# Kernel optimization log

Hardware: AMD Instinct MI355X
Metric: run time of the kernel (lower is better)

## Reference

```python
import jax, jax.numpy as jnp
import numpy as np

L, D, H, S, V, B = 8, 512, 8, 64, 66, 256
DH = D // H
EPS = 1e-10  # module's LayerNorm eps, added to std (not var)


def layernorm(x, g, b):
    # torch.std_mean default: unbiased std (ddof=1)
    mean = jnp.mean(x, axis=-1, keepdims=True)
    std = jnp.std(x, axis=-1, ddof=1, keepdims=True)
    return (x - mean) / (std + EPS) * g + b


def setup_inputs() -> dict:
    key = jax.random.key(0)
    ks = iter(jax.random.split(key, 32))
    def n(shape, scale=0.02):
        return jax.random.normal(next(ks), shape, dtype=jnp.float32) * scale
    return {
        "input_ids": jax.random.randint(next(ks), (B, S), 0, V),
        "targets": jax.random.randint(next(ks), (B, S), 0, V),
        "tok_emb": n((V, D), 1.0),
        "pos_emb": n((S, D), 1.0),
        "Wq": n((L, D, H, DH)), "Wk": n((L, D, H, DH)), "Wv": n((L, D, H, DH)),
        "Wo": n((L, D, D)), "bo": jnp.zeros((L, D), jnp.float32),
        "W1": n((L, D, 4 * D)), "b1": jnp.zeros((L, 4 * D), jnp.float32),
        "W2": n((L, 4 * D, D)), "b2": jnp.zeros((L, D), jnp.float32),
        "ln1_g": jnp.ones((L, D), jnp.float32), "ln1_b": jnp.zeros((L, D), jnp.float32),
        "ln2_g": jnp.ones((L, D), jnp.float32), "ln2_b": jnp.zeros((L, D), jnp.float32),
        "lnf_g": jnp.ones((D,), jnp.float32), "lnf_b": jnp.zeros((D,), jnp.float32),
        "Wu": n((D, V)), "bu": jnp.zeros((V,), jnp.float32),
    }


def reference(input_ids, targets, tok_emb, pos_emb, Wq, Wk, Wv, Wo, bo,
              W1, b1, W2, b2, ln1_g, ln1_b, ln2_g, ln2_b, lnf_g, lnf_b, Wu, bu):
    x = tok_emb[input_ids] + pos_emb[None, :, :]  # [B,S,D]
    scale = 1.0 / jnp.sqrt(jnp.float32(D))        # module scales by 1/sqrt(d_model)
    mask = jnp.tril(jnp.ones((S, S), dtype=bool))
    for l in range(L):
        h = layernorm(x, ln1_g[l], ln1_b[l])
        q = jnp.einsum('bsd,dhe->bhse', h, Wq[l])
        k = jnp.einsum('bsd,dhe->bhse', h, Wk[l])
        v = jnp.einsum('bsd,dhe->bhse', h, Wv[l])
        scores = jnp.einsum('bhse,bhte->bhst', q, k) * scale
        scores = jnp.where(mask, scores, -jnp.inf)
        attn = jax.nn.softmax(scores, axis=-1)
        o = jnp.einsum('bhst,bhte->bhse', attn, v)
        o = o.transpose(0, 2, 1, 3).reshape(B, S, D)  # concat heads (head order preserved)
        x = x + o @ Wo[l] + bo[l]
        h2 = layernorm(x, ln2_g[l], ln2_b[l])
        hid = jax.nn.gelu(h2 @ W1[l] + b1[l], approximate=False)  # nn.GELU exact
        x = x + hid @ W2[l] + b2[l]
    x = layernorm(x, lnf_g, lnf_b)
    logits = x @ Wu + bu  # [B,S,V]
    logp = jax.nn.log_softmax(logits, axis=-1)
    loss = -jnp.mean(jnp.take_along_axis(logp, targets[..., None], axis=-1))
    return logits, loss
```

## Files before the change

### kernel.cpp

```cpp
#include <hip/hip_runtime.h>
#include <hip/hip_bf16.h>
#include <math.h>

#define D_MODEL 512
#define NHEAD   8
#define DHEAD   64
#define SEQ     64
#define BATCH   256
#define NLAYER  8
#define VOCAB   66
#define FFDIM   2048
#define NTOK    (BATCH * SEQ)

typedef __attribute__((ext_vector_type(8))) short short8;
typedef __attribute__((ext_vector_type(4))) float f32x4;
typedef __attribute__((ext_vector_type(16))) float f32x16;

__device__ inline void async_copy16(const void* g, void* l) {
    __builtin_amdgcn_global_load_lds(
        (const __attribute__((address_space(1))) void*)g,
        (__attribute__((address_space(3))) void*)l,
        16, 0, 0);
}

__global__ __launch_bounds__(256) void transpose_conv(
        const float* __restrict__ W, __hip_bfloat16* __restrict__ Wt,
        int K, int M, size_t inLS, size_t outLS, int rowOff) {
    __shared__ float tile[32][33];
    int m0 = blockIdx.x * 32, k0 = blockIdx.y * 32;
    const float* Wl = W + blockIdx.z * inLS;
    __hip_bfloat16* Wtl = Wt + blockIdx.z * outLS;
    int t = threadIdx.x;
    #pragma unroll
    for (int p = 0; p < 4; p++) {
        int idx = t + p * 256;
        int kr = idx >> 5, mc = idx & 31;
        tile[kr][mc] = Wl[(size_t)(k0 + kr) * M + m0 + mc];
    }
    __syncthreads();
    #pragma unroll
    for (int p = 0; p < 4; p++) {
        int idx = t + p * 256;
        int mr = idx >> 5, kc = idx & 31;
        Wtl[(size_t)(rowOff + m0 + mr) * K + k0 + kc] = __float2bfloat16(tile[kc][mr]);
    }
}

__global__ __launch_bounds__(256) void conv_wu(
        const float* __restrict__ Wu, __hip_bfloat16* __restrict__ WuT) {
    int idx = blockIdx.x * 256 + threadIdx.x;
    int m = idx >> 9, k = idx & 511;
    WuT[idx] = __float2bfloat16(m < VOCAB ? Wu[(size_t)k * VOCAB + m] : 0.f);
}

__global__ void embed_kernel(const int* __restrict__ ids, const float* __restrict__ tok,
                             const float* __restrict__ pos, float* __restrict__ x) {
    int idx = blockIdx.x * 256 + threadIdx.x;
    int n = idx >> 9;
    int d = idx & 511;
    int s = n & (SEQ - 1);
    x[idx] = tok[ids[n] * D_MODEL + d] + pos[s * D_MODEL + d];
}

__global__ __launch_bounds__(256) void ln_kernel(
        const float* __restrict__ x, const float* __restrict__ g,
        const float* __restrict__ b, __hip_bfloat16* __restrict__ y) {
    int row = blockIdx.x * 4 + (threadIdx.x >> 6);
    int lane = threadIdx.x & 63;
    const float* xr = x + (size_t)row * D_MODEL + lane * 8;
    f32x4 v0 = *(const f32x4*)xr;
    f32x4 v1 = *(const f32x4*)(xr + 4);
    float s = 0.f, ss = 0.f;
    #pragma unroll
    for (int e = 0; e < 4; e++) { s += v0[e] + v1[e]; ss += v0[e] * v0[e] + v1[e] * v1[e]; }
    #pragma unroll
    for (int o = 1; o < 64; o <<= 1) {
        s  += __shfl_xor(s, o);
        ss += __shfl_xor(ss, o);
    }
    float mean = s / (float)D_MODEL;
    float var = (ss - (float)D_MODEL * mean * mean) / (float)(D_MODEL - 1);
    float denom = sqrtf(fmaxf(var, 0.f)) + 1e-10f;
    f32x4 g0 = *(const f32x4*)(g + lane * 8);
    f32x4 g1 = *(const f32x4*)(g + lane * 8 + 4);
    f32x4 b0 = *(const f32x4*)(b + lane * 8);
    f32x4 b1 = *(const f32x4*)(b + lane * 8 + 4);
    short8 outv;
    #pragma unroll
    for (int e = 0; e < 4; e++) {
        outv[e]     = ((__hip_bfloat16_raw)__float2bfloat16((v0[e] - mean) / denom * g0[e] + b0[e])).x;
        outv[e + 4] = ((__hip_bfloat16_raw)__float2bfloat16((v1[e] - mean) / denom * g1[e] + b1[e])).x;
    }
    *(short8*)((short*)y + (size_t)row * D_MODEL + lane * 8) = outv;
}

template <int ACT, int OUTMODE>
__global__ __launch_bounds__(256) void mfma_gemm(
        const __hip_bfloat16* __restrict__ A, const __hip_bfloat16* __restrict__ Bt,
        const float* __restrict__ bias, const float* addsrc,
        void* Cout, int K, int M, int ldc, int mstore) {
    __shared__ __align__(16) short As[128 * 64];
    __shared__ __align__(16) short Bs[128 * 64];
    int tid = threadIdx.x;
    int lane = tid & 63, wave = tid >> 6;
    int row0 = blockIdx.y * 128, col0 = blockIdx.x * 128;
    int wr = (wave >> 1) * 64, wc = (wave & 1) * 64;
    int l31 = lane & 31, h32 = lane >> 5;
    int l7 = l31 & 7;

    f32x16 acc[2][2] = {};

    int srow[4], skg[4];
    #pragma unroll
    for (int s = 0; s < 4; s++) {
        int u = s * 256 + tid;
        srow[s] = u >> 3;
        skg[s] = (u & 7) ^ (srow[s] & 7);
    }

    for (int k0 = 0; k0 < K; k0 += 64) {
        #pragma unroll
        for (int s = 0; s < 4; s++) {
            int u = s * 256 + tid;
            async_copy16((const short*)A + (size_t)(row0 + srow[s]) * K + k0 + skg[s] * 8,
                         As + u * 8);
            async_copy16((const short*)Bt + (size_t)(col0 + srow[s]) * K + k0 + skg[s] * 8,
                         Bs + u * 8);
        }
        __syncthreads();
        short8 af[2][4], bf[2][4];
        #pragma unroll
        for (int i = 0; i < 2; i++)
            #pragma unroll
            for (int kk = 0; kk < 4; kk++) {
                int kg = kk * 2 + h32;
                int c = kg ^ l7;
                af[i][kk] = *(const short8*)(As + ((wr + i * 32 + l31) * 8 + c) * 8);
                bf[i][kk] = *(const short8*)(Bs + ((wc + i * 32 + l31) * 8 + c) * 8);
            }
        #pragma unroll
        for (int i = 0; i < 2; i++)
            #pragma unroll
            for (int j = 0; j < 2; j++)
                #pragma unroll
                for (int kk = 0; kk < 4; kk++)
                    acc[i][j] = __builtin_amdgcn_mfma_f32_32x32x16_bf16(
                        af[i][kk], bf[j][kk], acc[i][j], 0, 0, 0);
        __syncthreads();
    }

    #pragma unroll
    for (int j = 0; j < 2; j++) {
        int col = col0 + wc + j * 32 + l31;
        if (OUTMODE == 2 && col >= mstore) continue;
        float bv = bias ? bias[col] : 0.f;
        #pragma unroll
        for (int i = 0; i < 2; i++) {
            int rbase = row0 + wr + i * 32 + 4 * h32;
            #pragma unroll
            for (int r = 0; r < 16; r++) {
                int row = rbase + (r & 3) + 8 * (r >> 2);
                float v = acc[i][j][r] + bv;
                if (OUTMODE == 1) v += addsrc[(size_t)row * M + col];
                if (ACT == 1) v = 0.5f * v * (1.f + erff(v * 0.70710678118654752f));
                if (OUTMODE == 0)
                    ((__hip_bfloat16*)Cout)[(size_t)row * M + col] = __float2bfloat16(v);
                else
                    ((float*)Cout)[(size_t)row * ldc + col] = v;
            }
        }
    }
}

#define PSTRIDE 72
__global__ __launch_bounds__(256) void attn_mfma(
        const __hip_bfloat16* __restrict__ QKV, __hip_bfloat16* __restrict__ O) {
    __shared__ __align__(16) short Vt[64 * PSTRIDE];
    __shared__ __align__(16) short P[64 * PSTRIDE];
    int bh = blockIdx.x;
    int b = bh >> 3, h = bh & 7;
    int t = threadIdx.x;
    int lane = t & 63, wave = t >> 6;
    int l15 = lane & 15, quad = lane >> 4;
    const float scale = 0.04419417382415922f;
    const short* base = (const short*)QKV + (size_t)(b * SEQ) * 1536 + h * DHEAD;

    {
        int j0 = (t >> 3) * 2;
        int c0 = (t & 7) * 8;
        const short* vrow = base + 1024 + (size_t)j0 * 1536 + c0;
        short8 va = *(const short8*)vrow;
        short8 vb = *(const short8*)(vrow + 1536);
        #pragma unroll
        for (int s = 0; s < 8; s++) {
            unsigned int packed = ((unsigned int)(unsigned short)vb[s] << 16) |
                                  (unsigned int)(unsigned short)va[s];
            *(unsigned int*)&Vt[(c0 + s) * PSTRIDE + j0] = packed;
        }
    }

    int r0 = wave * 16;
    short8 aq[2], bk[4][2];
    #pragma unroll
    for (int k = 0; k < 2; k++)
        aq[k] = *(const short8*)(base + (size_t)(r0 + l15) * 1536 + quad * 8 + 32 * k);
    #pragma unroll
    for (int j = 0; j < 4; j++)
        #pragma unroll
        for (int k = 0; k < 2; k++)
            bk[j][k] = *(const short8*)(base + 512 + (size_t)(j * 16 + l15) * 1536 + quad * 8 + 32 * k);

    f32x4 sc[4];
    #pragma unroll
    for (int j = 0; j < 4; j++) {
        f32x4 z = {};
        z = __builtin_amdgcn_mfma_f32_16x16x32_bf16(aq[0], bk[j][0], z, 0, 0, 0);
        sc[j] = __builtin_amdgcn_mfma_f32_16x16x32_bf16(aq[1], bk[j][1], z, 0, 0, 0);
    }

    float p[4][4];
    #pragma unroll
    for (int reg = 0; reg < 4; reg++) {
        int r = r0 + quad * 4 + reg;
        float m = -INFINITY;
        #pragma unroll
        for (int j = 0; j < 4; j++) {
            int c = j * 16 + l15;
            float s = (c <= r) ? sc[j][reg] * scale : -INFINITY;
            p[j][reg] = s;
            m = fmaxf(m, s);
        }
        #pragma unroll
        for (int o = 1; o < 16; o <<= 1) m = fmaxf(m, __shfl_xor(m, o));
        float sum = 0.f;
        #pragma unroll
        for (int j = 0; j < 4; j++) {
            float e = (p[j][reg] == -INFINITY) ? 0.f : expf(p[j][reg] - m);
            p[j][reg] = e;
            sum += e;
        }
        #pragma unroll
        for (int o = 1; o < 16; o <<= 1) sum += __shfl_xor(sum, o);
        float inv = 1.f / sum;
        #pragma unroll
        for (int j = 0; j < 4; j++) p[j][reg] *= inv;
    }

    #pragma unroll
    for (int j = 0; j < 4; j++)
        #pragma unroll
        for (int reg = 0; reg < 4; reg++) {
            int r = r0 + quad * 4 + reg;
            P[r * PSTRIDE + j * 16 + l15] =
                ((__hip_bfloat16_raw)__float2bfloat16(p[j][reg])).x;
        }

    __syncthreads();

    short8 ap[2];
    #pragma unroll
    for (int k = 0; k < 2; k++)
        ap[k] = *(const short8*)(P + (r0 + l15) * PSTRIDE + quad * 8 + 32 * k);
    #pragma unroll
    for (int jt = 0; jt < 4; jt++) {
        short8 bv0 = *(const short8*)(Vt + (jt * 16 + l15) * PSTRIDE + quad * 8);
        short8 bv1 = *(const short8*)(Vt + (jt * 16 + l15) * PSTRIDE + quad * 8 + 32);
        f32x4 o = {};
        o = __builtin_amdgcn_mfma_f32_16x16x32_bf16(ap[0], bv0, o, 0, 0, 0);
        o = __builtin_amdgcn_mfma_f32_16x16x32_bf16(ap[1], bv1, o, 0, 0, 0);
        #pragma unroll
        for (int reg = 0; reg < 4; reg++) {
            int r = r0 + quad * 4 + reg;
            int c = jt * 16 + l15;
            O[(size_t)(b * SEQ + r) * D_MODEL + h * DHEAD + c] = __float2bfloat16(o[reg]);
        }
    }
}

__global__ void zero_kernel(float* p) { if (threadIdx.x == 0) *p = 0.f; }

__global__ __launch_bounds__(256) void loss_kernel(
        const float* __restrict__ lg, const int* __restrict__ tgt,
        float* __restrict__ loss) {
    int wave = threadIdx.x >> 6;
    int l = threadIdx.x & 63;
    float local = 0.f;
    for (int row = blockIdx.x * 4 + wave; row < NTOK; row += gridDim.x * 4) {
        const float* lr = lg + (size_t)row * VOCAB;
        float a = lr[l];
        float bx = (l < VOCAB - 64) ? lr[64 + l] : -INFINITY;
        float m = fmaxf(a, bx);
        #pragma unroll
        for (int o = 32; o >= 1; o >>= 1) m = fmaxf(m, __shfl_xor(m, o));
        float s = expf(a - m) + ((l < VOCAB - 64) ? expf(bx - m) : 0.f);
        #pragma unroll
        for (int o = 32; o >= 1; o >>= 1) s += __shfl_xor(s, o);
        if (l == 0) local += lr[tgt[row]] - m - logf(s);
    }
    if (l == 0) atomicAdd(loss, -local / (float)NTOK);
}

extern "C" void kernel_launch(void* const* d_in, const int* in_sizes, int n_in,
                              void* d_out, int out_size, void* d_ws, size_t ws_size,
                              hipStream_t stream) {
    const int*   input_ids = (const int*)  d_in[0];
    const int*   targets   = (const int*)  d_in[1];
    const float* tok_emb   = (const float*)d_in[2];
    const float* pos_emb   = (const float*)d_in[3];
    const float* Wq        = (const float*)d_in[4];
    const float* Wk        = (const float*)d_in[5];
    const float* Wv        = (const float*)d_in[6];
    const float* Wo        = (const float*)d_in[7];
    const float* bo        = (const float*)d_in[8];
    const float* W1        = (const float*)d_in[9];
    const float* b1        = (const float*)d_in[10];
    const float* W2        = (const float*)d_in[11];
    const float* b2        = (const float*)d_in[12];
    const float* ln1_g     = (const float*)d_in[13];
    const float* ln1_b     = (const float*)d_in[14];
    const float* ln2_g     = (const float*)d_in[15];
    const float* ln2_b     = (const float*)d_in[16];
    const float* lnf_g     = (const float*)d_in[17];
    const float* lnf_b     = (const float*)d_in[18];
    const float* Wu        = (const float*)d_in[19];
    const float* bu        = (const float*)d_in[20];

    float* out  = (float*)d_out;
    float* loss = out + (size_t)NTOK * VOCAB;

    const size_t ND = (size_t)NTOK * D_MODEL;
    float* x             = (float*)d_ws;
    __hip_bfloat16* h    = (__hip_bfloat16*)(x + ND);
    __hip_bfloat16* qkv  = h + ND;
    __hip_bfloat16* ob   = qkv + 3 * ND;
    __hip_bfloat16* hid  = qkv;
    __hip_bfloat16* wqkvT = ob + ND;
    __hip_bfloat16* woT   = wqkvT + (size_t)NLAYER * 1536 * 512;
    __hip_bfloat16* w1T   = woT + (size_t)NLAYER * 512 * 512;
    __hip_bfloat16* w2T   = w1T + (size_t)NLAYER * 2048 * 512;
    __hip_bfloat16* wuT   = w2T + (size_t)NLAYER * 2048 * 512;

    transpose_conv<<<dim3(16, 16, NLAYER), 256, 0, stream>>>(Wq, wqkvT, 512, 512,
        (size_t)512 * 512, (size_t)1536 * 512, 0);
    transpose_conv<<<dim3(16, 16, NLAYER), 256, 0, stream>>>(Wk, wqkvT, 512, 512,
        (size_t)512 * 512, (size_t)1536 * 512, 512);
    transpose_conv<<<dim3(16, 16, NLAYER), 256, 0, stream>>>(Wv, wqkvT, 512, 512,
        (size_t)512 * 512, (size_t)1536 * 512, 1024);
    transpose_conv<<<dim3(16, 16, NLAYER), 256, 0, stream>>>(Wo, woT, 512, 512,
        (size_t)512 * 512, (size_t)512 * 512, 0);
    transpose_conv<<<dim3(64, 16, NLAYER), 256, 0, stream>>>(W1, w1T, 512, 2048,
        (size_t)512 * 2048, (size_t)2048 * 512, 0);
    transpose_conv<<<dim3(16, 64, NLAYER), 256, 0, stream>>>(W2, w2T, 2048, 512,
        (size_t)2048 * 512, (size_t)512 * 2048, 0);
    conv_wu<<<(128 * 512) / 256, 256, 0, stream>>>(Wu, wuT);

    embed_kernel<<<(NTOK * D_MODEL) / 256, 256, 0, stream>>>(input_ids, tok_emb, pos_emb, x);

    for (int l = 0; l < NLAYER; l++) {
        ln_kernel<<<NTOK / 4, 256, 0, stream>>>(x, ln1_g + l * D_MODEL, ln1_b + l * D_MODEL, h);
        mfma_gemm<0, 0><<<dim3(12, 128), 256, 0, stream>>>(
            h, wqkvT + (size_t)l * 1536 * 512, nullptr, nullptr, qkv, 512, 1536, 1536, 1536);
        attn_mfma<<<BATCH * NHEAD, 256, 0, stream>>>(qkv, ob);
        mfma_gemm<0, 1><<<dim3(4, 128), 256, 0, stream>>>(
            ob, woT + (size_t)l * 512 * 512, bo + l * D_MODEL, x, x, 512, 512, 512, 512);
        ln_kernel<<<NTOK / 4, 256, 0, stream>>>(x, ln2_g + l * D_MODEL, ln2_b + l * D_MODEL, h);
        mfma_gemm<1, 0><<<dim3(16, 128), 256, 0, stream>>>(
            h, w1T + (size_t)l * 2048 * 512, b1 + l * FFDIM, nullptr, hid, 512, 2048, 2048, 2048);
        mfma_gemm<0, 1><<<dim3(4, 128), 256, 0, stream>>>(
            hid, w2T + (size_t)l * 2048 * 512, b2 + l * D_MODEL, x, x, 2048, 512, 512, 512);
    }

    ln_kernel<<<NTOK / 4, 256, 0, stream>>>(x, lnf_g, lnf_b, h);
    mfma_gemm<0, 2><<<dim3(1, 128), 256, 0, stream>>>(
        h, wuT, bu, nullptr, out, 512, 128, VOCAB, VOCAB);
    zero_kernel<<<1, 64, 0, stream>>>(loss);
    loss_kernel<<<128, 256, 0, stream>>>(out, targets, loss);
}
```

Before: 2.115 ms.

## Add double-buffered GEMM staging only A in LDS, reading B from global

Adds a new GEMM kernel that double-buffers the A tile in LDS with async global-to-LDS copies, so the next K-slice loads while the current one computes. B fragments are read straight from global memory, no longer staged in LDS. The four per-layer GEMMs switch to this kernel, while the final unembedding GEMM keeps the old one. The aim is to overlap load latency with MFMA work and halve LDS traffic and barriers. The cost is uncoalesced, latency-exposed global reads of B on every k-step, which lean on the cache.

```diff
diff --git a/kernel.cpp b/kernel.cpp
--- a/kernel.cpp
+++ b/kernel.cpp
@@ -92,6 +92,86 @@
         outv[e + 4] = ((__hip_bfloat16_raw)__float2bfloat16((v1[e] - mean) / denom * g1[e] + b1[e])).x;
     }
     *(short8*)((short*)y + (size_t)row * D_MODEL + lane * 8) = outv;
+}
+
+template <int ACT, int OUTMODE>
+__global__ __launch_bounds__(256) void mfma_gemm2(
+        const __hip_bfloat16* __restrict__ A, const __hip_bfloat16* __restrict__ Bt,
+        const float* __restrict__ bias, const float* addsrc,
+        void* Cout, int K, int M) {
+    __shared__ __align__(16) short As[2][128 * 64];
+    int tid = threadIdx.x;
+    int lane = tid & 63, wave = tid >> 6;
+    int row0 = blockIdx.y * 128, col0 = blockIdx.x * 128;
+    int wr = (wave >> 1) * 64, wc = (wave & 1) * 64;
+    int l31 = lane & 31, h32 = lane >> 5;
+    int l7 = l31 & 7;
+
+    f32x16 acc[2][2] = {};
+
+    int srow[4], skg[4];
+    #pragma unroll
+    for (int s = 0; s < 4; s++) {
+        int u = s * 256 + tid;
+        srow[s] = u >> 3;
+        skg[s] = (u & 7) ^ (srow[s] & 7);
+    }
+
+    const short* Ab = (const short*)A + (size_t)row0 * K;
+    const short* Bg0 = (const short*)Bt + (size_t)(col0 + wc + l31) * K;
+    const short* Bg1 = (const short*)Bt + (size_t)(col0 + wc + 32 + l31) * K;
+
+    int niter = K >> 6;
+    #pragma unroll
+    for (int s = 0; s < 4; s++)
+        async_copy16(Ab + (size_t)srow[s] * K + skg[s] * 8, &As[0][(s * 256 + tid) * 8]);
+
+    for (int it = 0; it < niter; it++) {
+        __syncthreads();
+        if (it + 1 < niter) {
+            int k1 = (it + 1) << 6;
+            #pragma unroll
+            for (int s = 0; s < 4; s++)
+                async_copy16(Ab + (size_t)srow[s] * K + k1 + skg[s] * 8,
+                             &As[(it + 1) & 1][(s * 256 + tid) * 8]);
+        }
+        const short* Ac = &As[it & 1][0];
+        int k0 = it << 6;
+        #pragma unroll
+        for (int kk = 0; kk < 4; kk++) {
+            int kg = kk * 2 + h32;
+            int c = kg ^ l7;
+            short8 af0 = *(const short8*)(Ac + ((wr + l31) * 8 + c) * 8);
+            short8 af1 = *(const short8*)(Ac + ((wr + 32 + l31) * 8 + c) * 8);
+            short8 bf0 = *(const short8*)(Bg0 + k0 + kg * 8);
+            short8 bf1 = *(const short8*)(Bg1 + k0 + kg * 8);
+            acc[0][0] = __builtin_amdgcn_mfma_f32_32x32x16_bf16(af0, bf0, acc[0][0], 0, 0, 0);
+            acc[0][1] = __builtin_amdgcn_mfma_f32_32x32x16_bf16(af0, bf1, acc[0][1], 0, 0, 0);
+            acc[1][0] = __builtin_amdgcn_mfma_f32_32x32x16_bf16(af1, bf0, acc[1][0], 0, 0, 0);
+            acc[1][1] = __builtin_amdgcn_mfma_f32_32x32x16_bf16(af1, bf1, acc[1][1], 0, 0, 0);
+        }
+    }
+
+    #pragma unroll
+    for (int j = 0; j < 2; j++) {
+        int col = col0 + wc + j * 32 + l31;
+        float bv = bias ? bias[col] : 0.f;
+        #pragma unroll
+        for (int i = 0; i < 2; i++) {
+            int rbase = row0 + wr + i * 32 + 4 * h32;
+            #pragma unroll
+            for (int r = 0; r < 16; r++) {
+                int row = rbase + (r & 3) + 8 * (r >> 2);
+                float v = acc[i][j][r] + bv;
+                if (OUTMODE == 1) v += addsrc[(size_t)row * M + col];
+                if (ACT == 1) v = 0.5f * v * (1.f + erff(v * 0.70710678118654752f));
+                if (OUTMODE == 0)
+                    ((__hip_bfloat16*)Cout)[(size_t)row * M + col] = __float2bfloat16(v);
+                else
+                    ((float*)Cout)[(size_t)row * M + col] = v;
+            }
+        }
+    }
 }
 
 template <int ACT, int OUTMODE>
@@ -358,16 +438,16 @@
 
     for (int l = 0; l < NLAYER; l++) {
         ln_kernel<<<NTOK / 4, 256, 0, stream>>>(x, ln1_g + l * D_MODEL, ln1_b + l * D_MODEL, h);
-        mfma_gemm<0, 0><<<dim3(12, 128), 256, 0, stream>>>(
-            h, wqkvT + (size_t)l * 1536 * 512, nullptr, nullptr, qkv, 512, 1536, 1536, 1536);
+        mfma_gemm2<0, 0><<<dim3(12, 128), 256, 0, stream>>>(
+            h, wqkvT + (size_t)l * 1536 * 512, nullptr, nullptr, qkv, 512, 1536);
         attn_mfma<<<BATCH * NHEAD, 256, 0, stream>>>(qkv, ob);
-        mfma_gemm<0, 1><<<dim3(4, 128), 256, 0, stream>>>(
-            ob, woT + (size_t)l * 512 * 512, bo + l * D_MODEL, x, x, 512, 512, 512, 512);
+        mfma_gemm2<0, 1><<<dim3(4, 128), 256, 0, stream>>>(
+            ob, woT + (size_t)l * 512 * 512, bo + l * D_MODEL, x, x, 512, 512);
         ln_kernel<<<NTOK / 4, 256, 0, stream>>>(x, ln2_g + l * D_MODEL, ln2_b + l * D_MODEL, h);
-        mfma_gemm<1, 0><<<dim3(16, 128), 256, 0, stream>>>(
-            h, w1T + (size_t)l * 2048 * 512, b1 + l * FFDIM, nullptr, hid, 512, 2048, 2048, 2048);
-        mfma_gemm<0, 1><<<dim3(4, 128), 256, 0, stream>>>(
-            hid, w2T + (size_t)l * 2048 * 512, b2 + l * D_MODEL, x, x, 2048, 512, 512, 512);
+        mfma_gemm2<1, 0><<<dim3(16, 128), 256, 0, stream>>>(
+            h, w1T + (size_t)l * 2048 * 512, b1 + l * FFDIM, nullptr, hid, 512, 2048);
+        mfma_gemm2<0, 1><<<dim3(4, 128), 256, 0, stream>>>(
+            hid, w2T + (size_t)l * 2048 * 512, b2 + l * D_MODEL, x, x, 2048, 512);
     }
 
     ln_kernel<<<NTOK / 4, 256, 0, stream>>>(x, lnf_g, lnf_b, h);
```

Result: slower. 2.816 ms (+33.1%).

## Double-buffer LDS tiles in MFMA GEMM to overlap global loads with compute

Applied to the files above, without the earlier changes.

The bf16 MFMA GEMM now keeps two LDS buffers per operand. The next K-tile is prefetched with async global-to-LDS copies while the MFMAs run on the current one, and the trailing barrier per iteration is dropped. The goal is to hide global memory latency behind matrix math. In exchange, LDS per block doubles to 64KB, which may cut the number of resident blocks per CU.

```diff
diff --git a/kernel.cpp b/kernel.cpp
--- a/kernel.cpp
+++ b/kernel.cpp
@@ -99,8 +99,8 @@
         const __hip_bfloat16* __restrict__ A, const __hip_bfloat16* __restrict__ Bt,
         const float* __restrict__ bias, const float* addsrc,
         void* Cout, int K, int M, int ldc, int mstore) {
-    __shared__ __align__(16) short As[128 * 64];
-    __shared__ __align__(16) short Bs[128 * 64];
+    __shared__ __align__(16) short As[2][128 * 64];
+    __shared__ __align__(16) short Bs[2][128 * 64];
     int tid = threadIdx.x;
     int lane = tid & 63, wave = tid >> 6;
     int row0 = blockIdx.y * 128, col0 = blockIdx.x * 128;
@@ -118,16 +118,31 @@
         skg[s] = (u & 7) ^ (srow[s] & 7);
     }
 
-    for (int k0 = 0; k0 < K; k0 += 64) {
-        #pragma unroll
-        for (int s = 0; s < 4; s++) {
-            int u = s * 256 + tid;
-            async_copy16((const short*)A + (size_t)(row0 + srow[s]) * K + k0 + skg[s] * 8,
-                         As + u * 8);
-            async_copy16((const short*)Bt + (size_t)(col0 + srow[s]) * K + k0 + skg[s] * 8,
-                         Bs + u * 8);
-        }
+    const short* Ab = (const short*)A + (size_t)row0 * K;
+    const short* Bb = (const short*)Bt + (size_t)col0 * K;
+
+    int niter = K >> 6;
+    #pragma unroll
+    for (int s = 0; s < 4; s++) {
+        int u = s * 256 + tid;
+        async_copy16(Ab + (size_t)srow[s] * K + skg[s] * 8, &As[0][u * 8]);
+        async_copy16(Bb + (size_t)srow[s] * K + skg[s] * 8, &Bs[0][u * 8]);
+    }
+
+    for (int it = 0; it < niter; it++) {
         __syncthreads();
+        if (it + 1 < niter) {
+            int k1 = (it + 1) << 6;
+            int nb = (it + 1) & 1;
+            #pragma unroll
+            for (int s = 0; s < 4; s++) {
+                int u = s * 256 + tid;
+                async_copy16(Ab + (size_t)srow[s] * K + k1 + skg[s] * 8, &As[nb][u * 8]);
+                async_copy16(Bb + (size_t)srow[s] * K + k1 + skg[s] * 8, &Bs[nb][u * 8]);
+            }
+        }
+        const short* Ac = &As[it & 1][0];
+        const short* Bc = &Bs[it & 1][0];
         short8 af[2][4], bf[2][4];
         #pragma unroll
         for (int i = 0; i < 2; i++)
@@ -135,8 +150,8 @@
             for (int kk = 0; kk < 4; kk++) {
                 int kg = kk * 2 + h32;
                 int c = kg ^ l7;
-                af[i][kk] = *(const short8*)(As + ((wr + i * 32 + l31) * 8 + c) * 8);
-                bf[i][kk] = *(const short8*)(Bs + ((wc + i * 32 + l31) * 8 + c) * 8);
+                af[i][kk] = *(const short8*)(Ac + ((wr + i * 32 + l31) * 8 + c) * 8);
+                bf[i][kk] = *(const short8*)(Bc + ((wc + i * 32 + l31) * 8 + c) * 8);
             }
         #pragma unroll
         for (int i = 0; i < 2; i++)
@@ -146,7 +161,6 @@
                 for (int kk = 0; kk < 4; kk++)
                     acc[i][j] = __builtin_amdgcn_mfma_f32_32x32x16_bf16(
                         af[i][kk], bf[j][kk], acc[i][j], 0, 0, 0);
-        __syncthreads();
     }
 
     #pragma unroll
```

New measurement: 2.237 ms. 1.06x slower.
